# Kernel tuning notes

Measured on AMD Instinct MI355X. Metric: run time of the kernel, lower is better.

## Reference

```python
import jax, jax.numpy as jnp
import numpy as np

EPS = 1e-5  # BatchNorm eps
STRIDE = 10  # front_stride

def conv1d(x, w, b, stride=1, padding=0, dilation=1, groups=1):
    # x: [N,C,T], w: [O, C//groups, K] (torch OIH layout)
    y = jax.lax.conv_general_dilated(
        x, w, (stride,), [(padding, padding)], rhs_dilation=(dilation,),
        dimension_numbers=('NCH', 'OIH', 'NCH'), feature_group_count=groups)
    return y + b[None, :, None]

def bn_eval(x, g, b, m, v):
    scale = g / jnp.sqrt(v + EPS)
    return (x - m[None, :, None]) * scale[None, :, None] + b[None, :, None]

def prelu(x, a):
    return jnp.where(x > 0, x, a * x)

def setup_inputs() -> dict:
    key = jax.random.key(0)
    ks = jax.random.split(key, 12)
    B, Cin, T = 2, 1, 64000
    E, D, BL, L, K, FK = 256, 512, 2, 6, 3, 20
    s = 0.05
    x = jax.random.normal(ks[0], (B, Cin, T), dtype=jnp.float32)
    enc_w = jax.random.normal(ks[1], (E, Cin, FK), dtype=jnp.float32) * s
    enc_b = jnp.zeros((E,), jnp.float32)
    w1 = jax.random.normal(ks[2], (BL, L, D, E, 1), dtype=jnp.float32) * s
    b1 = jnp.zeros((BL, L, D), jnp.float32)
    a1 = jnp.full((BL, L), 0.25, jnp.float32)
    g1 = jnp.ones((BL, L, D), jnp.float32)
    be1 = jnp.zeros((BL, L, D), jnp.float32)
    m1 = jax.random.normal(ks[3], (BL, L, D), dtype=jnp.float32) * 0.1
    v1 = jax.random.uniform(ks[4], (BL, L, D), jnp.float32, 0.5, 1.5)
    wd = jax.random.normal(ks[5], (BL, L, D, 1, K), dtype=jnp.float32) * s
    bd = jnp.zeros((BL, L, D), jnp.float32)
    a2 = jnp.full((BL, L), 0.25, jnp.float32)
    g2 = jnp.ones((BL, L, D), jnp.float32)
    be2 = jnp.zeros((BL, L, D), jnp.float32)
    m2 = jax.random.normal(ks[6], (BL, L, D), dtype=jnp.float32) * 0.1
    v2 = jax.random.uniform(ks[7], (BL, L, D), jnp.float32, 0.5, 1.5)
    w2 = jax.random.normal(ks[8], (BL, L, E, D, 1), dtype=jnp.float32) * s
    b2 = jnp.zeros((BL, L, E), jnp.float32)
    dec_w = jax.random.normal(ks[9], (E, Cin, FK), dtype=jnp.float32) * s
    dec_b = jnp.zeros((Cin,), jnp.float32)
    return dict(x=x, enc_w=enc_w, enc_b=enc_b, w1=w1, b1=b1, a1=a1, g1=g1,
                be1=be1, m1=m1, v1=v1, wd=wd, bd=bd, a2=a2, g2=g2, be2=be2,
                m2=m2, v2=v2, w2=w2, b2=b2, dec_w=dec_w, dec_b=dec_b)

def reference(x, enc_w, enc_b, w1, b1, a1, g1, be1, m1, v1, wd, bd,
              a2, g2, be2, m2, v2, w2, b2, dec_w, dec_b):
    T = x.shape[2]
    FK = enc_w.shape[-1]
    D = wd.shape[2]
    blocks, layers = w1.shape[0], w1.shape[1]
    # encoder: Conv1d(in, E, FK, stride=10, padding=FK)
    enc = conv1d(x, enc_w, enc_b, stride=STRIDE, padding=FK)
    h = enc
    for bI in range(blocks):
        resid = h
        for i in range(layers):
            dil = 2 ** i
            h = conv1d(h, w1[bI, i], b1[bI, i])
            h = bn_eval(prelu(h, a1[bI, i]), g1[bI, i], be1[bI, i], m1[bI, i], v1[bI, i])
            h = conv1d(h, wd[bI, i], bd[bI, i], padding=dil, dilation=dil, groups=D)
            h = bn_eval(prelu(h, a2[bI, i]), g2[bI, i], be2[bI, i], m2[bI, i], v2[bI, i])
            h = conv1d(h, w2[bI, i], b2[bI, i])
        h = h + resid
    mask = jax.nn.sigmoid(h)
    masked = enc * mask
    # ConvTranspose1d(E, in, FK, stride=10, padding=0) as lhs-dilated conv
    wt = jnp.flip(dec_w, -1).transpose(1, 0, 2)  # [in, E, FK]
    dec = jax.lax.conv_general_dilated(
        masked, wt, (1,), [(FK - 1, FK - 1)], lhs_dilation=(STRIDE,),
        dimension_numbers=('NCH', 'OIH', 'NCH')) + dec_b[None, :, None]
    return dec[:, :, FK:T + FK]
```

## Files before the change

kernel.cpp:

```cpp
#include <hip/hip_runtime.h>
#include <math.h>

#define TLEN   64000
#define ECH    256
#define DCH    512
#define NBLK   2
#define NLAY   6
#define FKC    20
#define STRIDE_ 10
#define TC     6403
#define NS     12928
#define NTILE  101
#define EPSV   1e-5f

typedef __attribute__((ext_vector_type(8))) short          s8v;
typedef __attribute__((ext_vector_type(4))) float          f4v;
typedef __attribute__((ext_vector_type(4))) unsigned short u4v;
typedef __attribute__((ext_vector_type(8))) unsigned short u8v;

__device__ __forceinline__ unsigned short f2bf(float f) {
    union { float f; unsigned u; } v; v.f = f;
    unsigned r = v.u + 0x7FFFu + ((v.u >> 16) & 1u);
    return (unsigned short)(r >> 16);
}
__device__ __forceinline__ float bf2f(unsigned short h) {
    union { unsigned u; float f; } v; v.u = ((unsigned)h) << 16; return v.f;
}

__global__ __launch_bounds__(256)
void encoder_k(const float* __restrict__ x, const float* __restrict__ ew,
               const float* __restrict__ eb, float* __restrict__ enc,
               float* __restrict__ H)
{
    int n = blockIdx.x * 256 + threadIdx.x;
    int e = blockIdx.y;
    if (n >= NS) return;
    int b  = (n >= TC) ? 1 : 0;
    int tc = n - b * TC;
    float acc = 0.f;
    if (tc < TC) {
        acc = eb[e];
        const float* xb = x + b * TLEN;
        int base = tc * STRIDE_ - FKC;
        #pragma unroll
        for (int k = 0; k < FKC; ++k) {
            int idx = base + k;
            if (idx >= 0 && idx < TLEN) acc += xb[idx] * ew[e * FKC + k];
        }
    }
    enc[(size_t)e * NS + n] = acc;
    H[(size_t)e * NS + n]   = acc;
}

#define NWQ (12*512*256/4)
__global__ __launch_bounds__(256)
void wcvt_k(const float* __restrict__ w1, const float* __restrict__ w2,
            unsigned short* __restrict__ w1b, unsigned short* __restrict__ w2b)
{
    int i = blockIdx.x * 256 + threadIdx.x;
    if (i < NWQ) {
        float4 v = ((const float4*)w1)[i];
        u4v o = { f2bf(v.x), f2bf(v.y), f2bf(v.z), f2bf(v.w) };
        ((u4v*)w1b)[i] = o;
    } else {
        int j = i - NWQ;
        float4 v = ((const float4*)w2)[j];
        u4v o = { f2bf(v.x), f2bf(v.y), f2bf(v.z), f2bf(v.w) };
        ((u4v*)w2b)[j] = o;
    }
}

__global__ __launch_bounds__(256)
void t2b_k(const float* __restrict__ H32, unsigned short* __restrict__ Hb)
{
    __shared__ float ts[64][65];
    const int t  = threadIdx.x;
    const int n0 = blockIdx.x * 64;
    const int e0 = blockIdx.y * 64;
    const int nl = (t & 15) * 4;
    const int rr = t >> 4;
    #pragma unroll
    for (int r = 0; r < 4; ++r) {
        int er = rr + r * 16;
        float4 v = *(const float4*)&H32[(size_t)(e0 + er) * NS + n0 + nl];
        ts[er][nl + 0] = v.x; ts[er][nl + 1] = v.y;
        ts[er][nl + 2] = v.z; ts[er][nl + 3] = v.w;
    }
    __syncthreads();
    #pragma unroll
    for (int r = 0; r < 4; ++r) {
        int nr = rr + r * 16;
        u4v o = { f2bf(ts[nl + 0][nr]), f2bf(ts[nl + 1][nr]),
                  f2bf(ts[nl + 2][nr]), f2bf(ts[nl + 3][nr]) };
        *(u4v*)&Hb[(size_t)(n0 + nr) * 256 + e0 + nl] = o;
    }
}

#define LROW 40

template<int KD, int MOUT, int EPI, int OUTF>
__global__ __launch_bounds__(256)
void gemm_bf16_k(const unsigned short* __restrict__ Wb,
                 const unsigned short* __restrict__ Act,
                 unsigned short* __restrict__ OutB,
                 float* __restrict__ OutF,
                 const float* __restrict__ bias,
                 const float* __restrict__ alpha,
                 const float* __restrict__ gamma,
                 const float* __restrict__ beta,
                 const float* __restrict__ mean,
                 const float* __restrict__ var,
                 const unsigned short* __restrict__ Resid)
{
    __shared__ short At[128 * LROW];
    __shared__ short Bt[128 * LROW];

    const int t    = threadIdx.x;
    const int lane = t & 63;
    const int wid  = t >> 6;
    const int wm   = wid >> 1, wn = wid & 1;
    const int r16  = lane & 15, g = lane >> 4;
    const int mb   = blockIdx.y * 128;
    const int nb   = blockIdx.x * 128;

    const int arow = t >> 2;
    const int kc8  = (t & 3) * 8;

    f4v acc[4][4];
    #pragma unroll
    for (int a = 0; a < 4; ++a)
        #pragma unroll
        for (int c = 0; c < 4; ++c)
            acc[a][c] = (f4v){0.f, 0.f, 0.f, 0.f};

    for (int k0 = 0; k0 < KD; k0 += 32) {
        s8v a0 = *(const s8v*)&Wb[(size_t)(mb + arow)      * KD + k0 + kc8];
        s8v a1 = *(const s8v*)&Wb[(size_t)(mb + arow + 64) * KD + k0 + kc8];
        s8v b0 = *(const s8v*)&Act[(size_t)(nb + arow)      * KD + k0 + kc8];
        s8v b1 = *(const s8v*)&Act[(size_t)(nb + arow + 64) * KD + k0 + kc8];

        __syncthreads();
        *(s8v*)&At[(arow)      * LROW + kc8] = a0;
        *(s8v*)&At[(arow + 64) * LROW + kc8] = a1;
        *(s8v*)&Bt[(arow)      * LROW + kc8] = b0;
        *(s8v*)&Bt[(arow + 64) * LROW + kc8] = b1;
        __syncthreads();

        s8v av[4], bv[4];
        #pragma unroll
        for (int f = 0; f < 4; ++f) {
            av[f] = *(const s8v*)&At[(wm * 64 + f * 16 + r16) * LROW + g * 8];
            bv[f] = *(const s8v*)&Bt[(wn * 64 + f * 16 + r16) * LROW + g * 8];
        }
        #pragma unroll
        for (int fm = 0; fm < 4; ++fm)
            #pragma unroll
            for (int fn = 0; fn < 4; ++fn)
                acc[fm][fn] = __builtin_amdgcn_mfma_f32_16x16x32_bf16(
                    av[fm], bv[fn], acc[fm][fn], 0, 0, 0);
    }

    float al = 0.f;
    if constexpr (EPI == 0) al = alpha[0];
    #pragma unroll
    for (int fm = 0; fm < 4; ++fm) {
        const int mbase = mb + wm * 64 + fm * 16 + g * 4;
        float4 b4 = *(const float4*)&bias[mbase];
        float bb[4] = { b4.x, b4.y, b4.z, b4.w };
        float sc[4], mn[4], bt[4];
        if constexpr (EPI == 0) {
            float4 g4  = *(const float4*)&gamma[mbase];
            float4 v4  = *(const float4*)&var[mbase];
            float4 m4  = *(const float4*)&mean[mbase];
            float4 be4 = *(const float4*)&beta[mbase];
            sc[0] = g4.x / sqrtf(v4.x + EPSV); sc[1] = g4.y / sqrtf(v4.y + EPSV);
            sc[2] = g4.z / sqrtf(v4.z + EPSV); sc[3] = g4.w / sqrtf(v4.w + EPSV);
            mn[0] = m4.x; mn[1] = m4.y; mn[2] = m4.z; mn[3] = m4.w;
            bt[0] = be4.x; bt[1] = be4.y; bt[2] = be4.z; bt[3] = be4.w;
        }
        #pragma unroll
        for (int fn = 0; fn < 4; ++fn) {
            const int nloc = wn * 64 + fn * 16 + r16;
            const int n    = nb + nloc;
            f4v a = acc[fm][fn];
            u4v rv = {};
            if constexpr (EPI == 2) rv = *(const u4v*)&Resid[(size_t)n * MOUT + mbase];
            float y[4];
            #pragma unroll
            for (int r = 0; r < 4; ++r) {
                float v = a[r] + bb[r];
                if constexpr (EPI == 0) {
                    v = (v > 0.f) ? v : al * v;
                    v = (v - mn[r]) * sc[r] + bt[r];
                }
                if constexpr (EPI == 2) v += bf2f(rv[r]);
                y[r] = v;
            }
            if constexpr (OUTF == 0) {
                u4v ro = { f2bf(y[0]), f2bf(y[1]), f2bf(y[2]), f2bf(y[3]) };
                *(u4v*)&OutB[(size_t)n * MOUT + mbase] = ro;
            } else {
                #pragma unroll
                for (int r = 0; r < 4; ++r)
                    OutF[(size_t)(mbase + r) * NS + n] = y[r];
            }
        }
    }
}

__global__ __launch_bounds__(256)
void dw_k(const unsigned short* __restrict__ P, const float* __restrict__ wd,
          const float* __restrict__ bd, const float* __restrict__ a2,
          const float* __restrict__ g2, const float* __restrict__ be2,
          const float* __restrict__ m2, const float* __restrict__ v2,
          unsigned short* __restrict__ Q, int dil)
{
    const int t  = threadIdx.x;
    const int d8 = (t & 63) * 8;
    const int n  = blockIdx.x * 4 + (t >> 6);
    const int b  = (n >= TC) ? 1 : 0;
    const int tt = n - b * TC;

    u8v c = *(const u8v*)&P[(size_t)n * 512 + d8];
    u8v l = {}, r = {};
    const bool hasL = (tt - dil >= 0);
    const bool hasR = (tt + dil < TC);
    if (hasL) l = *(const u8v*)&P[(size_t)(n - dil) * 512 + d8];
    if (hasR) r = *(const u8v*)&P[(size_t)(n + dil) * 512 + d8];

    float w24[24];
    #pragma unroll
    for (int q = 0; q < 6; ++q) {
        float4 v = *(const float4*)&wd[d8 * 3 + q * 4];
        w24[q*4+0] = v.x; w24[q*4+1] = v.y; w24[q*4+2] = v.z; w24[q*4+3] = v.w;
    }
    float bdv[8], gv[8], bev[8], mnv[8], vrv[8];
    #pragma unroll
    for (int q = 0; q < 2; ++q) {
        float4 v0 = *(const float4*)&bd[d8 + q*4];
        float4 v1 = *(const float4*)&g2[d8 + q*4];
        float4 v2_ = *(const float4*)&be2[d8 + q*4];
        float4 v3 = *(const float4*)&m2[d8 + q*4];
        float4 v4 = *(const float4*)&v2[d8 + q*4];
        bdv[q*4+0]=v0.x; bdv[q*4+1]=v0.y; bdv[q*4+2]=v0.z; bdv[q*4+3]=v0.w;
        gv [q*4+0]=v1.x; gv [q*4+1]=v1.y; gv [q*4+2]=v1.z; gv [q*4+3]=v1.w;
        bev[q*4+0]=v2_.x;bev[q*4+1]=v2_.y;bev[q*4+2]=v2_.z;bev[q*4+3]=v2_.w;
        mnv[q*4+0]=v3.x; mnv[q*4+1]=v3.y; mnv[q*4+2]=v3.z; mnv[q*4+3]=v3.w;
        vrv[q*4+0]=v4.x; vrv[q*4+1]=v4.y; vrv[q*4+2]=v4.z; vrv[q*4+3]=v4.w;
    }
    const float al = a2[0];

    u8v o;
    #pragma unroll
    for (int i = 0; i < 8; ++i) {
        float acc = bf2f(c[i]) * w24[i*3+1];
        if (hasL) acc = fmaf(bf2f(l[i]), w24[i*3+0], acc);
        if (hasR) acc = fmaf(bf2f(r[i]), w24[i*3+2], acc);
        acc += bdv[i];
        acc = (acc > 0.f) ? acc : al * acc;
        acc = (acc - mnv[i]) * (gv[i] / sqrtf(vrv[i] + EPSV)) + bev[i];
        o[i] = f2bf(acc);
    }
    *(u8v*)&Q[(size_t)n * 512 + d8] = o;
}

__global__ __launch_bounds__(256)
void mask_k(const float* __restrict__ enc, const float* __restrict__ Hf,
            float* __restrict__ masked)
{
    size_t i = (size_t)blockIdx.x * 256 + threadIdx.x;
    if (i >= (size_t)ECH * NS) return;
    float hv = Hf[i];
    float s  = 1.f / (1.f + expf(-hv));
    masked[i] = enc[i] * s;
}

__global__ __launch_bounds__(256)
void decoder_k(const float* __restrict__ masked, const float* __restrict__ dw,
               const float* __restrict__ db, float* __restrict__ out)
{
    int t0 = blockIdx.x * 256 + threadIdx.x;
    int b  = blockIdx.y;
    if (t0 >= TLEN / STRIDE_) return;
    int tc0 = t0 + 2;
    float acc[10];
    #pragma unroll
    for (int j = 0; j < 10; ++j) acc[j] = 0.f;

    const float* mcol = masked + (size_t)b * TC + tc0;
    for (int e = 0; e < ECH; ++e) {
        float m0 = mcol[(size_t)e * NS];
        float m1 = mcol[(size_t)e * NS - 1];
        const float* wrow = dw + e * FKC;
        #pragma unroll
        for (int j = 0; j < 10; ++j)
            acc[j] = fmaf(m0, wrow[j], fmaf(m1, wrow[j + 10], acc[j]));
    }
    float bz = db[0];
    float* orow = out + (size_t)b * TLEN + t0 * 10;
    #pragma unroll
    for (int j = 0; j < 10; ++j) orow[j] = acc[j] + bz;
}

extern "C" void kernel_launch(void* const* d_in, const int* in_sizes, int n_in,
                              void* d_out, int out_size, void* d_ws, size_t ws_size,
                              hipStream_t stream)
{
    (void)in_sizes; (void)n_in; (void)out_size; (void)ws_size;
    const float* x     = (const float*)d_in[0];
    const float* enc_w = (const float*)d_in[1];
    const float* enc_b = (const float*)d_in[2];
    const float* w1    = (const float*)d_in[3];
    const float* b1    = (const float*)d_in[4];
    const float* a1    = (const float*)d_in[5];
    const float* g1    = (const float*)d_in[6];
    const float* be1   = (const float*)d_in[7];
    const float* m1    = (const float*)d_in[8];
    const float* v1    = (const float*)d_in[9];
    const float* wd    = (const float*)d_in[10];
    const float* bd    = (const float*)d_in[11];
    const float* a2    = (const float*)d_in[12];
    const float* g2    = (const float*)d_in[13];
    const float* be2   = (const float*)d_in[14];
    const float* m2    = (const float*)d_in[15];
    const float* v2    = (const float*)d_in[16];
    const float* w2    = (const float*)d_in[17];
    const float* b2    = (const float*)d_in[18];
    const float* dec_w = (const float*)d_in[19];
    const float* dec_b = (const float*)d_in[20];
    float* out = (float*)d_out;

    const size_t F_EN = (size_t)ECH * NS * 4;
    const size_t B_EN = (size_t)NS * 256 * 2;
    const size_t B_DN = (size_t)NS * 512 * 2;
    char* p = (char*)d_ws;
    float*          H32   = (float*)p;           p += F_EN;
    float*          enc32 = (float*)p;           p += F_EN;
    unsigned short* Hb    = (unsigned short*)p;  p += B_EN;
    unsigned short* Rb    = (unsigned short*)p;  p += B_EN;
    unsigned short* Pb    = (unsigned short*)p;  p += B_DN;
    unsigned short* Qb    = (unsigned short*)p;  p += B_DN;
    unsigned short* w1b   = (unsigned short*)p;  p += (size_t)12*512*256*2;
    unsigned short* w2b   = (unsigned short*)p;
    float* masked = (float*)Pb;

    dim3 blk(256);
    wcvt_k<<<dim3(2 * NWQ / 256), blk, 0, stream>>>(w1, w2, w1b, w2b);
    encoder_k<<<dim3((NS + 255) / 256, ECH), blk, 0, stream>>>(x, enc_w, enc_b, enc32, H32);
    t2b_k<<<dim3(NS / 64, ECH / 64), blk, 0, stream>>>(H32, Hb);

    for (int bI = 0; bI < NBLK; ++bI) {
        hipMemcpyAsync(Rb, Hb, B_EN, hipMemcpyDeviceToDevice, stream);
        for (int i = 0; i < NLAY; ++i) {
            const int li  = bI * NLAY + i;
            const int dil = 1 << i;
            gemm_bf16_k<ECH, DCH, 0, 0><<<dim3(NTILE, 4), blk, 0, stream>>>(
                w1b + (size_t)li * DCH * ECH, Hb, Pb, nullptr,
                b1 + (size_t)li * DCH, a1 + li,
                g1 + (size_t)li * DCH, be1 + (size_t)li * DCH,
                m1 + (size_t)li * DCH, v1 + (size_t)li * DCH, nullptr);
            dw_k<<<dim3(NS / 4), blk, 0, stream>>>(
                Pb, wd + (size_t)li * DCH * 3, bd + (size_t)li * DCH, a2 + li,
                g2 + (size_t)li * DCH, be2 + (size_t)li * DCH,
                m2 + (size_t)li * DCH, v2 + (size_t)li * DCH, Qb, dil);
            if (li == NBLK * NLAY - 1) {
                gemm_bf16_k<DCH, ECH, 2, 1><<<dim3(NTILE, 2), blk, 0, stream>>>(
                    w2b + (size_t)li * ECH * DCH, Qb, nullptr, H32,
                    b2 + (size_t)li * ECH, nullptr, nullptr, nullptr,
                    nullptr, nullptr, Rb);
            } else if (i == NLAY - 1) {
                gemm_bf16_k<DCH, ECH, 2, 0><<<dim3(NTILE, 2), blk, 0, stream>>>(
                    w2b + (size_t)li * ECH * DCH, Qb, Hb, nullptr,
                    b2 + (size_t)li * ECH, nullptr, nullptr, nullptr,
                    nullptr, nullptr, Rb);
            } else {
                gemm_bf16_k<DCH, ECH, 1, 0><<<dim3(NTILE, 2), blk, 0, stream>>>(
                    w2b + (size_t)li * ECH * DCH, Qb, Hb, nullptr,
                    b2 + (size_t)li * ECH, nullptr, nullptr, nullptr,
                    nullptr, nullptr, nullptr);
            }
        }
    }

    size_t totE = (size_t)ECH * NS;
    mask_k<<<dim3((unsigned)((totE + 255) / 256)), blk, 0, stream>>>(enc32, H32, masked);
    decoder_k<<<dim3(TLEN / STRIDE_ / 256 + ((TLEN / STRIDE_ % 256) ? 1 : 0), NBLK),
                blk, 0, stream>>>(masked, dec_w, dec_b, out);
}
```

Baseline: 781.1 us.

## Move encoder/mask/decoder to bf16 token-major layout and prefetch GEMM tiles

```diff
diff --git a/kernel.cpp b/kernel.cpp
--- a/kernel.cpp
+++ b/kernel.cpp
@@ -27,31 +27,6 @@
     union { unsigned u; float f; } v; v.u = ((unsigned)h) << 16; return v.f;
 }
 
-__global__ __launch_bounds__(256)
-void encoder_k(const float* __restrict__ x, const float* __restrict__ ew,
-               const float* __restrict__ eb, float* __restrict__ enc,
-               float* __restrict__ H)
-{
-    int n = blockIdx.x * 256 + threadIdx.x;
-    int e = blockIdx.y;
-    if (n >= NS) return;
-    int b  = (n >= TC) ? 1 : 0;
-    int tc = n - b * TC;
-    float acc = 0.f;
-    if (tc < TC) {
-        acc = eb[e];
-        const float* xb = x + b * TLEN;
-        int base = tc * STRIDE_ - FKC;
-        #pragma unroll
-        for (int k = 0; k < FKC; ++k) {
-            int idx = base + k;
-            if (idx >= 0 && idx < TLEN) acc += xb[idx] * ew[e * FKC + k];
-        }
-    }
-    enc[(size_t)e * NS + n] = acc;
-    H[(size_t)e * NS + n]   = acc;
-}
-
 #define NWQ (12*512*256/4)
 __global__ __launch_bounds__(256)
 void wcvt_k(const float* __restrict__ w1, const float* __restrict__ w2,
@@ -71,39 +46,49 @@
 }
 
 __global__ __launch_bounds__(256)
-void t2b_k(const float* __restrict__ H32, unsigned short* __restrict__ Hb)
-{
-    __shared__ float ts[64][65];
-    const int t  = threadIdx.x;
-    const int n0 = blockIdx.x * 64;
-    const int e0 = blockIdx.y * 64;
-    const int nl = (t & 15) * 4;
-    const int rr = t >> 4;
-    #pragma unroll
-    for (int r = 0; r < 4; ++r) {
-        int er = rr + r * 16;
-        float4 v = *(const float4*)&H32[(size_t)(e0 + er) * NS + n0 + nl];
-        ts[er][nl + 0] = v.x; ts[er][nl + 1] = v.y;
-        ts[er][nl + 2] = v.z; ts[er][nl + 3] = v.w;
+void encoder_k(const float* __restrict__ x, const float* __restrict__ ew,
+               const float* __restrict__ eb,
+               unsigned short* __restrict__ EncB, unsigned short* __restrict__ Hb)
+{
+    __shared__ float xs[660];
+    const int bx  = blockIdx.x;
+    const int b   = blockIdx.y;
+    const int tc0 = bx * 64;
+    const int base_g = tc0 * STRIDE_ - FKC;
+    for (int i = threadIdx.x; i < 660; i += 256) {
+        int idx = base_g + i;
+        xs[i] = (idx >= 0 && idx < TLEN) ? x[b * TLEN + idx] : 0.f;
     }
     __syncthreads();
-    #pragma unroll
-    for (int r = 0; r < 4; ++r) {
-        int nr = rr + r * 16;
-        u4v o = { f2bf(ts[nl + 0][nr]), f2bf(ts[nl + 1][nr]),
-                  f2bf(ts[nl + 2][nr]), f2bf(ts[nl + 3][nr]) };
-        *(u4v*)&Hb[(size_t)(n0 + nr) * 256 + e0 + nl] = o;
+
+    const int e = threadIdx.x;
+    float w[20];
+    #pragma unroll
+    for (int q = 0; q < 5; ++q) {
+        float4 v = *(const float4*)&ew[e * 20 + q * 4];
+        w[q*4+0] = v.x; w[q*4+1] = v.y; w[q*4+2] = v.z; w[q*4+3] = v.w;
+    }
+    const float bz = eb[e];
+    const int jmax = (TC - tc0 < 64) ? (TC - tc0) : 64;
+    for (int j = 0; j < jmax; ++j) {
+        const float* xp = &xs[j * 10];
+        float acc = bz;
+        #pragma unroll
+        for (int k = 0; k < 20; ++k) acc = fmaf(xp[k], w[k], acc);
+        unsigned short hv = f2bf(acc);
+        size_t o = (size_t)(b * TC + tc0 + j) * 256 + e;
+        EncB[o] = hv;
+        Hb[o]   = hv;
     }
 }
 
 #define LROW 40
 
-template<int KD, int MOUT, int EPI, int OUTF>
+template<int KD, int MOUT, int EPI>
 __global__ __launch_bounds__(256)
 void gemm_bf16_k(const unsigned short* __restrict__ Wb,
                  const unsigned short* __restrict__ Act,
                  unsigned short* __restrict__ OutB,
-                 float* __restrict__ OutF,
                  const float* __restrict__ bias,
                  const float* __restrict__ alpha,
                  const float* __restrict__ gamma,
@@ -126,6 +111,11 @@
     const int arow = t >> 2;
     const int kc8  = (t & 3) * 8;
 
+    const unsigned short* pA0 = &Wb[(size_t)(mb + arow)      * KD + kc8];
+    const unsigned short* pA1 = &Wb[(size_t)(mb + arow + 64) * KD + kc8];
+    const unsigned short* pB0 = &Act[(size_t)(nb + arow)      * KD + kc8];
+    const unsigned short* pB1 = &Act[(size_t)(nb + arow + 64) * KD + kc8];
+
     f4v acc[4][4];
     #pragma unroll
     for (int a = 0; a < 4; ++a)
@@ -133,12 +123,13 @@
         for (int c = 0; c < 4; ++c)
             acc[a][c] = (f4v){0.f, 0.f, 0.f, 0.f};
 
-    for (int k0 = 0; k0 < KD; k0 += 32) {
-        s8v a0 = *(const s8v*)&Wb[(size_t)(mb + arow)      * KD + k0 + kc8];
-        s8v a1 = *(const s8v*)&Wb[(size_t)(mb + arow + 64) * KD + k0 + kc8];
-        s8v b0 = *(const s8v*)&Act[(size_t)(nb + arow)      * KD + k0 + kc8];
-        s8v b1 = *(const s8v*)&Act[(size_t)(nb + arow + 64) * KD + k0 + kc8];
-
+    constexpr int NSTEP = KD / 32;
+    s8v a0 = *(const s8v*)(pA0);
+    s8v a1 = *(const s8v*)(pA1);
+    s8v b0 = *(const s8v*)(pB0);
+    s8v b1 = *(const s8v*)(pB1);
+
+    for (int s = 0; s < NSTEP; ++s) {
         __syncthreads();
         *(s8v*)&At[(arow)      * LROW + kc8] = a0;
         *(s8v*)&At[(arow + 64) * LROW + kc8] = a1;
@@ -146,6 +137,12 @@
         *(s8v*)&Bt[(arow + 64) * LROW + kc8] = b1;
         __syncthreads();
 
+        const int k0n = ((s + 1 < NSTEP) ? (s + 1) : s) * 32;
+        s8v na0 = *(const s8v*)(pA0 + k0n);
+        s8v na1 = *(const s8v*)(pA1 + k0n);
+        s8v nb0 = *(const s8v*)(pB0 + k0n);
+        s8v nb1 = *(const s8v*)(pB1 + k0n);
+
         s8v av[4], bv[4];
         #pragma unroll
         for (int f = 0; f < 4; ++f) {
@@ -158,6 +155,8 @@
             for (int fn = 0; fn < 4; ++fn)
                 acc[fm][fn] = __builtin_amdgcn_mfma_f32_16x16x32_bf16(
                     av[fm], bv[fn], acc[fm][fn], 0, 0, 0);
+
+        a0 = na0; a1 = na1; b0 = nb0; b1 = nb1;
     }
 
     float al = 0.f;
@@ -180,12 +179,11 @@
         }
         #pragma unroll
         for (int fn = 0; fn < 4; ++fn) {
-            const int nloc = wn * 64 + fn * 16 + r16;
-            const int n    = nb + nloc;
+            const int n = nb + wn * 64 + fn * 16 + r16;
             f4v a = acc[fm][fn];
             u4v rv = {};
             if constexpr (EPI == 2) rv = *(const u4v*)&Resid[(size_t)n * MOUT + mbase];
-            float y[4];
+            u4v ro;
             #pragma unroll
             for (int r = 0; r < 4; ++r) {
                 float v = a[r] + bb[r];
@@ -194,16 +192,9 @@
                     v = (v - mn[r]) * sc[r] + bt[r];
                 }
                 if constexpr (EPI == 2) v += bf2f(rv[r]);
-                y[r] = v;
+                ro[r] = f2bf(v);
             }
-            if constexpr (OUTF == 0) {
-                u4v ro = { f2bf(y[0]), f2bf(y[1]), f2bf(y[2]), f2bf(y[3]) };
-                *(u4v*)&OutB[(size_t)n * MOUT + mbase] = ro;
-            } else {
-                #pragma unroll
-                for (int r = 0; r < 4; ++r)
-                    OutF[(size_t)(mbase + r) * NS + n] = y[r];
-            }
+            *(u4v*)&OutB[(size_t)n * MOUT + mbase] = ro;
         }
     }
 }
@@ -264,42 +255,75 @@
     *(u8v*)&Q[(size_t)n * 512 + d8] = o;
 }
 
-__global__ __launch_bounds__(256)
-void mask_k(const float* __restrict__ enc, const float* __restrict__ Hf,
-            float* __restrict__ masked)
-{
-    size_t i = (size_t)blockIdx.x * 256 + threadIdx.x;
-    if (i >= (size_t)ECH * NS) return;
-    float hv = Hf[i];
-    float s  = 1.f / (1.f + expf(-hv));
-    masked[i] = enc[i] * s;
-}
-
-__global__ __launch_bounds__(256)
-void decoder_k(const float* __restrict__ masked, const float* __restrict__ dw,
-               const float* __restrict__ db, float* __restrict__ out)
-{
-    int t0 = blockIdx.x * 256 + threadIdx.x;
-    int b  = blockIdx.y;
-    if (t0 >= TLEN / STRIDE_) return;
-    int tc0 = t0 + 2;
+#define TOT8 ((ECH * NS) / 8)
+__global__ __launch_bounds__(256)
+void mask_k(const unsigned short* __restrict__ EncB,
+            const unsigned short* __restrict__ Hb,
+            unsigned short* __restrict__ Mb)
+{
+    int i = blockIdx.x * 256 + threadIdx.x;
+    u8v ev = ((const u8v*)EncB)[i];
+    u8v hv = ((const u8v*)Hb)[i];
+    u8v o;
+    #pragma unroll
+    for (int k = 0; k < 8; ++k) {
+        float h = bf2f(hv[k]);
+        float s = 1.f / (1.f + expf(-h));
+        o[k] = f2bf(bf2f(ev[k]) * s);
+    }
+    ((u8v*)Mb)[i] = o;
+}
+
+__global__ __launch_bounds__(256)
+void decoder_k(const unsigned short* __restrict__ Mb,
+               const float* __restrict__ dec_w, const float* __restrict__ db,
+               float* __restrict__ out)
+{
+    __shared__ float wlds[5120];
+    __shared__ float red[2560];
+    const int t = threadIdx.x;
+    #pragma unroll
+    for (int i = 0; i < 5; ++i)
+        ((float4*)wlds)[t + i * 256] = ((const float4*)dec_w)[t + i * 256];
+    __syncthreads();
+
+    const int grp = t >> 5;
+    const int t0l = t & 31;
+    const int t0  = blockIdx.x * 32 + t0l;
+    const int by  = blockIdx.y;
+    const int n0  = by * TC + t0 + 2;
+    const int e0  = grp * 32;
+
     float acc[10];
     #pragma unroll
     for (int j = 0; j < 10; ++j) acc[j] = 0.f;
 
-    const float* mcol = masked + (size_t)b * TC + tc0;
-    for (int e = 0; e < ECH; ++e) {
-        float m0 = mcol[(size_t)e * NS];
-        float m1 = mcol[(size_t)e * NS - 1];
-        const float* wrow = dw + e * FKC;
-        #pragma unroll
-        for (int j = 0; j < 10; ++j)
-            acc[j] = fmaf(m0, wrow[j], fmaf(m1, wrow[j + 10], acc[j]));
-    }
-    float bz = db[0];
-    float* orow = out + (size_t)b * TLEN + t0 * 10;
-    #pragma unroll
-    for (int j = 0; j < 10; ++j) orow[j] = acc[j] + bz;
+    #pragma unroll
+    for (int q = 0; q < 4; ++q) {
+        u8v a0 = *(const u8v*)&Mb[(size_t)n0 * 256 + e0 + q * 8];
+        u8v a1 = *(const u8v*)&Mb[(size_t)(n0 - 1) * 256 + e0 + q * 8];
+        #pragma unroll
+        for (int i = 0; i < 8; ++i) {
+            float m0 = bf2f(a0[i]);
+            float m1 = bf2f(a1[i]);
+            const float* wr = &wlds[(e0 + q * 8 + i) * 20];
+            #pragma unroll
+            for (int j = 0; j < 10; ++j)
+                acc[j] = fmaf(m0, wr[j], fmaf(m1, wr[j + 10], acc[j]));
+        }
+    }
+    #pragma unroll
+    for (int j = 0; j < 10; ++j)
+        red[(t0l * 8 + grp) * 10 + j] = acc[j];
+    __syncthreads();
+
+    for (int s = t; s < 320; s += 256) {
+        int t0l2 = s / 10, j = s - t0l2 * 10;
+        float sm = 0.f;
+        #pragma unroll
+        for (int gq = 0; gq < 8; ++gq) sm += red[(t0l2 * 8 + gq) * 10 + j];
+        out[(size_t)by * TLEN + (size_t)(blockIdx.x * 32 + t0l2) * 10 + j] = sm + db[0];
+    }
 }
 
 extern "C" void kernel_launch(void* const* d_in, const int* in_sizes, int n_in,
@@ -330,32 +354,29 @@
     const float* dec_b = (const float*)d_in[20];
     float* out = (float*)d_out;
 
-    const size_t F_EN = (size_t)ECH * NS * 4;
     const size_t B_EN = (size_t)NS * 256 * 2;
     const size_t B_DN = (size_t)NS * 512 * 2;
     char* p = (char*)d_ws;
-    float*          H32   = (float*)p;           p += F_EN;
-    float*          enc32 = (float*)p;           p += F_EN;
-    unsigned short* Hb    = (unsigned short*)p;  p += B_EN;
-    unsigned short* Rb    = (unsigned short*)p;  p += B_EN;
-    unsigned short* Pb    = (unsigned short*)p;  p += B_DN;
-    unsigned short* Qb    = (unsigned short*)p;  p += B_DN;
-    unsigned short* w1b   = (unsigned short*)p;  p += (size_t)12*512*256*2;
-    unsigned short* w2b   = (unsigned short*)p;
-    float* masked = (float*)Pb;
+    unsigned short* Hb   = (unsigned short*)p;  p += B_EN;
+    unsigned short* Hb2  = (unsigned short*)p;  p += B_EN;
+    unsigned short* EncB = (unsigned short*)p;  p += B_EN;
+    unsigned short* Pb   = (unsigned short*)p;  p += B_DN;
+    unsigned short* Qb   = (unsigned short*)p;  p += B_DN;
+    unsigned short* w1b  = (unsigned short*)p;  p += (size_t)12*512*256*2;
+    unsigned short* w2b  = (unsigned short*)p;
+    unsigned short* Mb   = Pb;
 
     dim3 blk(256);
     wcvt_k<<<dim3(2 * NWQ / 256), blk, 0, stream>>>(w1, w2, w1b, w2b);
-    encoder_k<<<dim3((NS + 255) / 256, ECH), blk, 0, stream>>>(x, enc_w, enc_b, enc32, H32);
-    t2b_k<<<dim3(NS / 64, ECH / 64), blk, 0, stream>>>(H32, Hb);
+    encoder_k<<<dim3(101, 2), blk, 0, stream>>>(x, enc_w, enc_b, EncB, Hb);
 
     for (int bI = 0; bI < NBLK; ++bI) {
-        hipMemcpyAsync(Rb, Hb, B_EN, hipMemcpyDeviceToDevice, stream);
         for (int i = 0; i < NLAY; ++i) {
             const int li  = bI * NLAY + i;
             const int dil = 1 << i;
-            gemm_bf16_k<ECH, DCH, 0, 0><<<dim3(NTILE, 4), blk, 0, stream>>>(
-                w1b + (size_t)li * DCH * ECH, Hb, Pb, nullptr,
+            const unsigned short* hin = (i == 0) ? Hb : Hb2;
+            gemm_bf16_k<ECH, DCH, 0><<<dim3(NTILE, 4), blk, 0, stream>>>(
+                w1b + (size_t)li * DCH * ECH, hin, Pb,
                 b1 + (size_t)li * DCH, a1 + li,
                 g1 + (size_t)li * DCH, be1 + (size_t)li * DCH,
                 m1 + (size_t)li * DCH, v1 + (size_t)li * DCH, nullptr);
@@ -363,27 +384,20 @@
                 Pb, wd + (size_t)li * DCH * 3, bd + (size_t)li * DCH, a2 + li,
                 g2 + (size_t)li * DCH, be2 + (size_t)li * DCH,
                 m2 + (size_t)li * DCH, v2 + (size_t)li * DCH, Qb, dil);
-            if (li == NBLK * NLAY - 1) {
-                gemm_bf16_k<DCH, ECH, 2, 1><<<dim3(NTILE, 2), blk, 0, stream>>>(
-                    w2b + (size_t)li * ECH * DCH, Qb, nullptr, H32,
+            if (i == NLAY - 1) {
+                gemm_bf16_k<DCH, ECH, 2><<<dim3(NTILE, 2), blk, 0, stream>>>(
+                    w2b + (size_t)li * ECH * DCH, Qb, Hb,
                     b2 + (size_t)li * ECH, nullptr, nullptr, nullptr,
-                    nullptr, nullptr, Rb);
-            } else if (i == NLAY - 1) {
-                gemm_bf16_k<DCH, ECH, 2, 0><<<dim3(NTILE, 2), blk, 0, stream>>>(
-                    w2b + (size_t)li * ECH * DCH, Qb, Hb, nullptr,
-                    b2 + (size_t)li * ECH, nullptr, nullptr, nullptr,
-                    nullptr, nullptr, Rb);
+                    nullptr, nullptr, Hb);
             } else {
-                gemm_bf16_k<DCH, ECH, 1, 0><<<dim3(NTILE, 2), blk, 0, stream>>>(
-                    w2b + (size_t)li * ECH * DCH, Qb, Hb, nullptr,
+                gemm_bf16_k<DCH, ECH, 1><<<dim3(NTILE, 2), blk, 0, stream>>>(
+                    w2b + (size_t)li * ECH * DCH, Qb, Hb2,
                     b2 + (size_t)li * ECH, nullptr, nullptr, nullptr,
                     nullptr, nullptr, nullptr);
             }
         }
     }
 
-    size_t totE = (size_t)ECH * NS;
-    mask_k<<<dim3((unsigned)((totE + 255) / 256)), blk, 0, stream>>>(enc32, H32, masked);
-    decoder_k<<<dim3(TLEN / STRIDE_ / 256 + ((TLEN / STRIDE_ % 256) ? 1 : 0), NBLK),
-                blk, 0, stream>>>(masked, dec_w, dec_b, out);
-}
+    mask_k<<<dim3(TOT8 / 256), blk, 0, stream>>>(EncB, Hb, Mb);
+    decoder_k<<<dim3(200, 2), blk, 0, stream>>>(Mb, dec_w, dec_b, out);
+}
```

New measurement: 643.7 us. 17.6% less time.
